# Kernel tuning notes

Measured on AMD Instinct MI355X. Metric: run time of the kernel, lower is better.

Reference implementation:

```python
import jax, jax.numpy as jnp
import numpy as np

EPS = 1e-6
NHEAD = 12

def _ln(x):
    m = jnp.mean(x, -1, keepdims=True)
    v = jnp.var(x, -1, keepdims=True)
    return (x - m) * jax.lax.rsqrt(v + EPS)

def _modulate(x, shift, scale):
    return x * (1 + scale[:, None, :]) + shift[:, None, :]

def _pos_embedding(idx, dim, max_len=2048):
    K = jnp.arange(dim // 2)
    ang = idx[..., None] * jnp.pi / (max_len ** (2.0 * K / dim))
    return jnp.concatenate([jnp.sin(ang), jnp.cos(ang)], axis=-1)

def _forward(x, W_xemb, b_xemb, ds_table, sg_table, Wqkv, bqkv, Wo, bo, W1, b1, W2, b2,
             Wada, bada, Wada_f, bada_f, W_out, dataset, spacegroup, mask):
    B, N, _ = x.shape
    D = W_xemb.shape[1]
    hd = D // NHEAD
    # conditioning vector: label embeddings (eval mode: no cfg dropout)
    c = ds_table[dataset] + sg_table[spacegroup]                 # [B, D]
    h = x @ W_xemb + b_xemb + _pos_embedding(jnp.arange(N), D)[None]  # [B, N, D]
    kmask = mask[:, None, None, :]                                # [B,1,1,N], True = padded key
    scale_qk = 1.0 / jnp.sqrt(jnp.asarray(hd, h.dtype))

    def block(h, p):
        Wqkv, bqkv, Wo, bo, W1, b1, W2, b2, Wada, bada = p
        mods = jax.nn.silu(c) @ Wada + bada                      # [B, 6D]
        sh_a, sc_a, g_a, sh_m, sc_m, g_m = jnp.split(mods, 6, axis=-1)
        xm = _modulate(_ln(h), sh_a, sc_a)
        qkv = (xm @ Wqkv + bqkv).reshape(B, N, 3, NHEAD, hd)
        q, k, v = qkv[:, :, 0], qkv[:, :, 1], qkv[:, :, 2]
        scores = jnp.einsum('bqhd,bkhd->bhqk', q, k) * scale_qk   # MATH-backend path: full [B,H,N,N]
        scores = jnp.where(kmask, -jnp.inf, scores)
        attn = jax.nn.softmax(scores, axis=-1)
        o = jnp.einsum('bhqk,bkhd->bqhd', attn, v).reshape(B, N, D)
        o = o @ Wo + bo
        h = h + g_a[:, None, :] * o
        y = _modulate(_ln(h), sh_m, sc_m)
        y = jax.nn.gelu(y @ W1 + b1, approximate=True) @ W2 + b2
        h = h + g_m[:, None, :] * y
        return h, None

    h, _ = jax.lax.scan(block, h, (Wqkv, bqkv, Wo, bo, W1, b1, W2, b2, Wada, bada))
    mods_f = jax.nn.silu(c) @ Wada_f + bada_f
    sh_f, sc_f = jnp.split(mods_f, 2, axis=-1)
    return _modulate(_ln(h), sh_f, sc_f) @ W_out                  # [B, N, 1] per-token energy


def setup_inputs() -> dict:
    B, N, D, L, DX, HID = 32, 512, 768, 12, 8, 3072
    keys = iter(jax.random.split(jax.random.key(0), 32))
    def w(shape, s=0.02):
        return jax.random.normal(next(keys), shape, jnp.float32) * s
    return dict(
        x=jax.random.normal(next(keys), (B, N, 2 * DX), jnp.float32),
        W_xemb=w((2 * DX, D)), b_xemb=jnp.zeros((D,), jnp.float32),
        ds_table=w((3, D)), sg_table=w((231, D)),
        Wqkv=w((L, D, 3 * D)), bqkv=jnp.zeros((L, 3 * D), jnp.float32),
        Wo=w((L, D, D)), bo=jnp.zeros((L, D), jnp.float32),
        W1=w((L, D, HID)), b1=jnp.zeros((L, HID), jnp.float32),
        W2=w((L, HID, D)), b2=jnp.zeros((L, D), jnp.float32),
        Wada=w((L, D, 6 * D)), bada=jnp.zeros((L, 6 * D), jnp.float32),
        Wada_f=w((D, 2 * D)), bada_f=jnp.zeros((2 * D,), jnp.float32),
        W_out=w((D, 1)),
        dataset=jax.random.randint(next(keys), (32,), 0, 2),
        spacegroup=jax.random.randint(next(keys), (32,), 0, 230),
        mask=jax.random.bernoulli(next(keys), 0.1, (32, 512)),
    )


def reference(x, W_xemb, b_xemb, ds_table, sg_table, Wqkv, bqkv, Wo, bo, W1, b1, W2, b2,
              Wada, bada, Wada_f, bada_f, W_out, dataset, spacegroup, mask):
    return _forward(x, W_xemb, b_xemb, ds_table, sg_table, Wqkv, bqkv, Wo, bo, W1, b1,
                    W2, b2, Wada, bada, Wada_f, bada_f, W_out, dataset, spacegroup, mask)
```

## Files before the change

### kernel.cpp

```cpp
#include <hip/hip_runtime.h>
#include <hip/hip_bf16.h>

#define B_   32
#define N_   512
#define D_   768
#define H_   12
#define HID_ 3072
#define L_   12
#define M_   (B_*N_)

typedef __attribute__((ext_vector_type(8))) short short8_t;
typedef __attribute__((ext_vector_type(4))) short short4_t;
typedef __attribute__((ext_vector_type(4))) float f32x4;
typedef __hip_bfloat16 bf16;

__device__ __forceinline__ void gll16(const void* g, void* l){
    __builtin_amdgcn_global_load_lds((const __attribute__((address_space(1))) void*)g,
                                     (__attribute__((address_space(3))) void*)l, 16, 0, 0);
}

__global__ __launch_bounds__(256) void embed_kernel(
    const float* __restrict__ x, const float* __restrict__ Wx,
    const float* __restrict__ bx, float* __restrict__ h)
{
    long idx = (long)blockIdx.x * 256 + threadIdx.x;
    int d = (int)(idx % 768);
    long m = idx / 768;
    int n = (int)(m % 512);
    float acc = bx[d];
    const float* xr = x + m * 16;
    #pragma unroll
    for (int k = 0; k < 16; ++k) acc = fmaf(xr[k], Wx[k*768 + d], acc);
    int K = (d < 384) ? d : d - 384;
    float ang = (float)n * 3.14159265358979323846f * expf(-(2.0f*(float)K/768.0f) * 7.624618986159398f);
    acc += (d < 384) ? sinf(ang) : cosf(ang);
    h[idx] = acc;
}

__global__ __launch_bounds__(256) void csilu_kernel(
    const float* __restrict__ ds_t, const float* __restrict__ sg_t,
    const int* __restrict__ dataset, const int* __restrict__ sg, float* __restrict__ out)
{
    int idx = blockIdx.x*256 + threadIdx.x;
    int b = idx / 768, d = idx % 768;
    float c = ds_t[dataset[b]*768 + d] + sg_t[sg[b]*768 + d];
    out[idx] = c / (1.0f + expf(-c));
}

__global__ __launch_bounds__(256) void mods_part_kernel(
    const float* __restrict__ csilu, const float* __restrict__ W,
    float* __restrict__ part, int Nd2, long wLayerStride)
{
    __shared__ float cs[16][96];
    int n2 = blockIdx.x*256 + threadIdx.x;
    int l = blockIdx.y, z = blockIdx.z;
    int kz = z >> 1, bg = z & 1;
    int L = gridDim.y;
    for (int t = threadIdx.x; t < 16*96; t += 256){
        int bb = t / 96, kk = t - bb*96;
        cs[bb][kk] = csilu[(bg*16 + bb)*768 + kz*96 + kk];
    }
    __syncthreads();
    const float2* Wl = (const float2*)(W + (long)l*wLayerStride);
    float2 acc[16];
    #pragma unroll
    for (int b=0;b<16;b++) acc[b] = make_float2(0.f, 0.f);
    for (int k=0;k<96;++k){
        float2 wv = Wl[(long)(kz*96 + k)*Nd2 + n2];
        #pragma unroll
        for (int b=0;b<16;b++){
            float c = cs[b][k];
            acc[b].x = fmaf(c, wv.x, acc[b].x);
            acc[b].y = fmaf(c, wv.y, acc[b].y);
        }
    }
    float2* pp = (float2*)part + ((long)(kz*L + l)*32 + bg*16)*Nd2 + n2;
    #pragma unroll
    for (int b=0;b<16;b++) pp[(long)b*Nd2] = acc[b];
}

__global__ __launch_bounds__(256) void mods_reduce_kernel(
    const float* __restrict__ part, const float* __restrict__ bias,
    float* __restrict__ out, int Nd, int L)
{
    long idx = (long)blockIdx.x*256 + threadIdx.x;
    int n = (int)(idx % Nd);
    long r = idx / Nd;
    int b = (int)(r & 31);
    int l = (int)(r >> 5);
    float s = bias[(long)l*Nd + n];
    #pragma unroll
    for (int z=0;z<8;z++) s += part[((long)(z*L + l)*32 + b)*Nd + n];
    out[idx] = s;
}

__global__ __launch_bounds__(256) void transpose4_kernel(
    const float* __restrict__ Wqkv, const float* __restrict__ Wo,
    const float* __restrict__ W1,  const float* __restrict__ W2,
    bf16* __restrict__ wqT, bf16* __restrict__ woT,
    bf16* __restrict__ w1T, bf16* __restrict__ w2T)
{
    __shared__ float t[32][33];
    int tt = blockIdx.x;
    const float* src; bf16* dst; int K, Nd, nx;
    if (tt < 1728){ src=Wqkv; dst=wqT; K=768; Nd=2304; nx=72; }
    else if (tt < 2304){ src=Wo; dst=woT; K=768; Nd=768; nx=24; tt -= 1728; }
    else if (tt < 4608){ src=W1; dst=w1T; K=768; Nd=3072; nx=96; tt -= 2304; }
    else { src=W2; dst=w2T; K=3072; Nd=768; nx=24; tt -= 4608; }
    int n0 = (tt % nx)*32, k0 = (tt / nx)*32;
    int tx = threadIdx.x & 31, ty = threadIdx.x >> 5;
    #pragma unroll
    for (int j=0;j<4;j++)
        t[ty + j*8][tx] = src[(long)(k0 + ty + j*8)*Nd + n0 + tx];
    __syncthreads();
    #pragma unroll
    for (int j=0;j<4;j++)
        dst[(long)(n0 + ty + j*8)*K + k0 + tx] = __float2bfloat16(t[tx][ty + j*8]);
}

__global__ __launch_bounds__(256) void ln_mod_kernel(
    const float* __restrict__ h, const float* __restrict__ shiftB,
    const float* __restrict__ scaleB, int modsStride, bf16* __restrict__ out)
{
    int wave = threadIdx.x >> 6, lane = threadIdx.x & 63;
    long row = (long)blockIdx.x*4 + wave;
    int b = (int)(row >> 9);
    const float4* xr = (const float4*)(h + row*768);
    float4 v[3];
    float s = 0.f, ss = 0.f;
    #pragma unroll
    for (int i=0;i<3;i++){
        v[i] = xr[lane + i*64];
        s  += v[i].x + v[i].y + v[i].z + v[i].w;
        ss += v[i].x*v[i].x + v[i].y*v[i].y + v[i].z*v[i].z + v[i].w*v[i].w;
    }
    #pragma unroll
    for (int o=1;o<64;o<<=1){ s += __shfl_xor(s,o,64); ss += __shfl_xor(ss,o,64); }
    float mean = s * (1.0f/768.0f);
    float var  = ss * (1.0f/768.0f) - mean*mean;
    float rstd = rsqrtf(var + 1e-6f);
    const float4* sh4 = (const float4*)(shiftB + (long)b*modsStride);
    const float4* sc4 = (const float4*)(scaleB + (long)b*modsStride);
    short4_t* orow = (short4_t*)(out + row*768);
    #pragma unroll
    for (int i=0;i<3;i++){
        float4 sh = sh4[lane + i*64];
        float4 sc = sc4[lane + i*64];
        float o0 = (v[i].x-mean)*rstd*(1.f+sc.x) + sh.x;
        float o1 = (v[i].y-mean)*rstd*(1.f+sc.y) + sh.y;
        float o2 = (v[i].z-mean)*rstd*(1.f+sc.z) + sh.z;
        float o3 = (v[i].w-mean)*rstd*(1.f+sc.w) + sh.w;
        bf16 b0 = __float2bfloat16(o0), b1 = __float2bfloat16(o1);
        bf16 b2 = __float2bfloat16(o2), b3 = __float2bfloat16(o3);
        short4_t pk;
        pk[0] = *(short*)&b0; pk[1] = *(short*)&b1;
        pk[2] = *(short*)&b2; pk[3] = *(short*)&b3;
        orow[lane + i*64] = pk;
    }
}

__device__ __forceinline__ float gelu_f(float x){
    float z2 = 1.5957691216057308f * x * (1.0f + 0.044715f*x*x);
    return x / (1.0f + __expf(-z2));
}

template<int MODE>
__global__ __launch_bounds__(256, 2) void gemm128_kernel(
    const bf16* __restrict__ A, const bf16* __restrict__ Bw,
    const float* __restrict__ bias, bf16* __restrict__ outBf,
    float* __restrict__ hres, const float* __restrict__ gate,
    int Nd, int Kd, int gateStride)
{
    __shared__ __align__(16) short lds[40960];
    int tid = threadIdx.x;
    int lane = tid & 63, wave = tid >> 6;
    int frow = lane & 15, g = lane >> 4;

    int nx = gridDim.x;
    int bid = blockIdx.y * nx + blockIdx.x;
    int xcd = bid & 7;
    int wq  = bid >> 3;
    int mt  = xcd * 16 + (wq & 15);
    int ct  = wq >> 4;
    int m0 = mt * 128, n0 = ct * 192;
    int wn = wave * 48;

    const short* Ag = (const short*)A;
    const short* Bg = (const short*)Bw;
    int r0 = tid >> 3, s0 = (tid & 7) ^ ((tid >> 3) & 7);
    const short* aSrc = Ag + (long)(m0 + r0)*Kd + s0*8;
    const short* bSrc = Bg + (long)(n0 + r0)*Kd + s0*8;
    long rj = (long)32*Kd;
    int wbase = wave*512;

    int aFrag = frow*64;
    int bFrag = (wn + frow)*64;
    int slotK0 = (g ^ (frow & 7))*8;
    int slotK1 = ((4+g) ^ (frow & 7))*8;

    f32x4 acc[8][3];
    #pragma unroll
    for (int i=0;i<8;i++)
        #pragma unroll
        for (int j=0;j<3;j++) acc[i][j] = (f32x4){0.f,0.f,0.f,0.f};

    int NT = Kd >> 6;

#define STAGE(kt, ps) { \
    int par_ = (kt)&1; \
    if ((ps)==0){ \
        short* d_ = &lds[par_*8192 + wbase]; \
        gll16(aSrc +        (long)(kt)*64, d_); \
        gll16(aSrc +   rj + (long)(kt)*64, d_ + 2048); \
        gll16(aSrc + 2*rj + (long)(kt)*64, d_ + 4096); \
        gll16(aSrc + 3*rj + (long)(kt)*64, d_ + 6144); \
    } else { \
        short* d_ = &lds[16384 + par_*12288 + wbase]; \
        gll16(bSrc +        (long)(kt)*64, d_); \
        gll16(bSrc +   rj + (long)(kt)*64, d_ + 2048); \
        gll16(bSrc + 2*rj + (long)(kt)*64, d_ + 4096); \
        gll16(bSrc + 3*rj + (long)(kt)*64, d_ + 6144); \
        gll16(bSrc + 4*rj + (long)(kt)*64, d_ + 8192); \
        gll16(bSrc + 5*rj + (long)(kt)*64, d_ + 10240); \
    } }

    STAGE(0,0); STAGE(0,1);

    for (int kt=0; kt<NT; ++kt){
        int pA  = (kt&1)*8192;
        int pBb = 16384 + (kt&1)*12288;
        bool pf = (kt+1 < NT);
        if (pf){
            STAGE(kt+1, 0);
            asm volatile("s_waitcnt vmcnt(4)" ::: "memory");
        } else {
            asm volatile("s_waitcnt vmcnt(0)" ::: "memory");
        }
        __builtin_amdgcn_s_barrier();
        __builtin_amdgcn_sched_barrier(0);
        if (pf) STAGE(kt+1, 1);
        short8_t af0[8], af1[8], bf0[3], bf1[3];
        #pragma unroll
        for (int i=0;i<8;i++){
            af0[i] = *(const short8_t*)&lds[pA + aFrag + i*1024 + slotK0];
            af1[i] = *(const short8_t*)&lds[pA + aFrag + i*1024 + slotK1];
        }
        #pragma unroll
        for (int j=0;j<3;j++){
            bf0[j] = *(const short8_t*)&lds[pBb + bFrag + j*1024 + slotK0];
            bf1[j] = *(const short8_t*)&lds[pBb + bFrag + j*1024 + slotK1];
        }
        __builtin_amdgcn_s_setprio(1);
        #pragma unroll
        for (int i=0;i<8;i++)
            #pragma unroll
            for (int j=0;j<3;j++)
                acc[i][j] = __builtin_amdgcn_mfma_f32_16x16x32_bf16(af0[i], bf0[j], acc[i][j], 0, 0, 0);
        #pragma unroll
        for (int i=0;i<8;i++)
            #pragma unroll
            for (int j=0;j<3;j++)
                acc[i][j] = __builtin_amdgcn_mfma_f32_16x16x32_bf16(af1[i], bf1[j], acc[i][j], 0, 0, 0);
        __builtin_amdgcn_s_setprio(0);
        __builtin_amdgcn_sched_barrier(0);
        __builtin_amdgcn_s_barrier();
        __builtin_amdgcn_sched_barrier(0);
    }
#undef STAGE

    int rbase = m0 + g*4;
    int cbase = n0 + wn + frow;
    float bv0 = bias[cbase], bv1 = bias[cbase+16], bv2 = bias[cbase+32];
    #pragma unroll
    for (int i=0;i<8;i++){
        #pragma unroll
        for (int r=0;r<4;r++){
            int row = rbase + i*16 + r;
            float v0 = acc[i][0][r] + bv0;
            float v1 = acc[i][1][r] + bv1;
            float v2 = acc[i][2][r] + bv2;
            if (MODE == 0){
                bf16* o_ = outBf + (long)row*Nd + cbase;
                o_[0]  = __float2bfloat16(v0);
                o_[16] = __float2bfloat16(v1);
                o_[32] = __float2bfloat16(v2);
            } else if (MODE == 1){
                bf16* o_ = outBf + (long)row*Nd + cbase;
                o_[0]  = __float2bfloat16(gelu_f(v0));
                o_[16] = __float2bfloat16(gelu_f(v1));
                o_[32] = __float2bfloat16(gelu_f(v2));
            } else {
                int bb = row >> 9;
                const float* gp = gate + (long)bb*gateStride + cbase;
                float* hp = hres + (long)row*768 + cbase;
                hp[0]  += gp[0]  * v0;
                hp[16] += gp[16] * v1;
                hp[32] += gp[32] * v2;
            }
        }
    }
}

__global__ __launch_bounds__(256) void attn_mfma_kernel(
    const bf16* __restrict__ qkv, const int* __restrict__ mask, bf16* __restrict__ o)
{
    __shared__ __align__(16) short Ks[64][72];
    __shared__ __align__(16) short Vt[64][72];
    __shared__ __align__(16) short Ps[4][16][72];
    __shared__ float maskf[512];
    int tid = threadIdx.x, lane = tid & 63, wave = tid >> 6;
    int qt = blockIdx.x, hh = blockIdx.y, b = blockIdx.z;
    long base = (long)b * 512 * 2304;
    const short* qkvs = (const short*)qkv;

    maskf[tid]       = mask[b*512 + tid]       ? -1e30f : 0.0f;
    maskf[tid + 256] = mask[b*512 + tid + 256] ? -1e30f : 0.0f;

    int c = lane & 15, g = lane >> 4;
    int qrowA = qt*64 + wave*16 + c;
    const short* qptr = qkvs + base + (long)qrowA*2304 + hh*64 + g*8;
    short8_t qa0 = *(const short8_t*)qptr;
    short8_t qa1 = *(const short8_t*)(qptr + 32);

    f32x4 oacc[4];
    #pragma unroll
    for (int j=0;j<4;j++) oacc[j] = (f32x4){0.f,0.f,0.f,0.f};
    float m_r[4], l_r[4];
    #pragma unroll
    for (int r=0;r<4;r++){ m_r[r] = -50.0f; l_r[r] = 0.0f; }

    int kp = (tid & 31)*2, gv = tid >> 5;
    const short* kgbase = qkvs + base + 768  + hh*64;
    const short* vgbase = qkvs + base + 1536 + hh*64 + gv*8;

    for (int kt=0; kt<8; ++kt){
        __syncthreads();
        {
            int v0 = tid, v1 = tid + 256;
            int r0 = v0>>3, c0 = (v0&7)*8, r1 = v1>>3, c1 = (v1&7)*8;
            *(short8_t*)&Ks[r0][c0] = *(const short8_t*)(kgbase + (long)(kt*64 + r0)*2304 + c0);
            *(short8_t*)&Ks[r1][c1] = *(const short8_t*)(kgbase + (long)(kt*64 + r1)*2304 + c1);
            short8_t va = *(const short8_t*)(vgbase + (long)(kt*64 + kp    )*2304);
            short8_t vb = *(const short8_t*)(vgbase + (long)(kt*64 + kp + 1)*2304);
            #pragma unroll
            for (int e=0;e<8;e++){
                unsigned int pack = (unsigned int)(unsigned short)va[e]
                                  | ((unsigned int)(unsigned short)vb[e] << 16);
                *(unsigned int*)&Vt[gv*8 + e][kp] = pack;
            }
        }
        __syncthreads();
        f32x4 s[4];
        #pragma unroll
        for (int j=0;j<4;j++){
            short8_t kb0 = *(const short8_t*)&Ks[j*16 + c][g*8];
            short8_t kb1 = *(const short8_t*)&Ks[j*16 + c][g*8 + 32];
            f32x4 z = (f32x4){0.f,0.f,0.f,0.f};
            z = __builtin_amdgcn_mfma_f32_16x16x32_bf16(qa0, kb0, z, 0, 0, 0);
            z = __builtin_amdgcn_mfma_f32_16x16x32_bf16(qa1, kb1, z, 0, 0, 0);
            s[j] = z;
        }
        #pragma unroll
        for (int j=0;j<4;j++){
            float mbj = maskf[kt*64 + j*16 + c];
            #pragma unroll
            for (int r=0;r<4;r++) s[j][r] = s[j][r]*0.125f + mbj;
        }
        #pragma unroll
        for (int r=0;r<4;r++){
            float tm = fmaxf(fmaxf(s[0][r], s[1][r]), fmaxf(s[2][r], s[3][r]));
            #pragma unroll
            for (int o_=1;o_<16;o_<<=1) tm = fmaxf(tm, __shfl_xor(tm, o_, 64));
            float mn  = fmaxf(m_r[r], tm);
            float fac = __expf(m_r[r] - mn);
            m_r[r] = mn;
            float ls = l_r[r]*fac;
            #pragma unroll
            for (int j=0;j<4;j++){
                float p = __expf(s[j][r] - mn);
                s[j][r] = p;
                ls += p;
            }
            l_r[r] = ls;
            #pragma unroll
            for (int j=0;j<4;j++) oacc[j][r] *= fac;
        }
        #pragma unroll
        for (int j=0;j<4;j++)
            #pragma unroll
            for (int r=0;r<4;r++)
                *(bf16*)&Ps[wave][g*4 + r][j*16 + c] = __float2bfloat16(s[j][r]);
        short8_t pa0 = *(const short8_t*)&Ps[wave][c][g*8];
        short8_t pa1 = *(const short8_t*)&Ps[wave][c][g*8 + 32];
        #pragma unroll
        for (int j=0;j<4;j++){
            short8_t vb0 = *(const short8_t*)&Vt[j*16 + c][g*8];
            short8_t vb1 = *(const short8_t*)&Vt[j*16 + c][g*8 + 32];
            oacc[j] = __builtin_amdgcn_mfma_f32_16x16x32_bf16(pa0, vb0, oacc[j], 0, 0, 0);
            oacc[j] = __builtin_amdgcn_mfma_f32_16x16x32_bf16(pa1, vb1, oacc[j], 0, 0, 0);
        }
    }
    #pragma unroll
    for (int r=0;r<4;r++){
        float lt = l_r[r];
        #pragma unroll
        for (int o_=1;o_<16;o_<<=1) lt += __shfl_xor(lt, o_, 64);
        l_r[r] = 1.0f / lt;
    }
    int qrowC = qt*64 + wave*16 + g*4;
    bf16* orow = o + ((long)b*512 + qrowC)*768 + hh*64;
    #pragma unroll
    for (int r=0;r<4;r++)
        #pragma unroll
        for (int j=0;j<4;j++)
            orow[(long)r*768 + j*16 + c] = __float2bfloat16(oacc[j][r] * l_r[r]);
}

__global__ __launch_bounds__(256) void outdot_kernel(
    const bf16* __restrict__ xm, const float* __restrict__ Wout, float* __restrict__ out)
{
    int tid=threadIdx.x, lane=tid&63, wave=tid>>6;
    long row = (long)blockIdx.x*4 + wave;
    const bf16* xr = xm + row*768;
    float acc = 0.f;
    #pragma unroll
    for (int i=0;i<12;i++){ int d = lane + i*64; acc = fmaf(__bfloat162float(xr[d]), Wout[d], acc); }
    #pragma unroll
    for (int o_=1;o_<64;o_<<=1) acc += __shfl_xor(acc, o_, 64);
    if (lane==0) out[row] = acc;
}

extern "C" void kernel_launch(void* const* d_in, const int* in_sizes, int n_in,
                              void* d_out, int out_size, void* d_ws, size_t ws_size,
                              hipStream_t stream)
{
    const float* x      = (const float*)d_in[0];
    const float* W_xemb = (const float*)d_in[1];
    const float* b_xemb = (const float*)d_in[2];
    const float* ds_t   = (const float*)d_in[3];
    const float* sg_t   = (const float*)d_in[4];
    const float* Wqkv   = (const float*)d_in[5];
    const float* bqkv   = (const float*)d_in[6];
    const float* Wo     = (const float*)d_in[7];
    const float* bo     = (const float*)d_in[8];
    const float* W1     = (const float*)d_in[9];
    const float* b1     = (const float*)d_in[10];
    const float* W2     = (const float*)d_in[11];
    const float* b2     = (const float*)d_in[12];
    const float* Wada   = (const float*)d_in[13];
    const float* bada   = (const float*)d_in[14];
    const float* Wada_f = (const float*)d_in[15];
    const float* bada_f = (const float*)d_in[16];
    const float* W_out  = (const float*)d_in[17];
    const int* dataset  = (const int*)d_in[18];
    const int* sgroup   = (const int*)d_in[19];
    const int* mask     = (const int*)d_in[20];
    float* out = (float*)d_out;

    char* ws = (char*)d_ws;
    size_t off = 0;
    auto alloc = [&](size_t bytes)->void*{
        void* p = ws + off; off += (bytes + 255) & ~(size_t)255; return p; };
    float* h     = (float*)alloc((size_t)M_*768*4);
    float* csilu = (float*)alloc((size_t)32*768*4);
    float* modsA = (float*)alloc((size_t)12*32*4608*4);
    float* modsF = (float*)alloc((size_t)32*1536*4);
    bf16*  xm    = (bf16*) alloc((size_t)M_*768*2);
    bf16*  wbuf  = (bf16*) alloc((size_t)7077888*2);
    bf16*  big   = (bf16*) alloc((size_t)M_*3072*2);
    bf16* qkvb = big;
    bf16* y1   = big;
    float* partA = (float*)big;
    float* partF = partA + (size_t)8*12*32*4608;
    bf16* wqT = wbuf;
    bf16* woT = wqT + 2304*768;
    bf16* w1T = woT + 768*768;
    bf16* w2T = w1T + 3072*768;

    embed_kernel<<<49152, 256, 0, stream>>>(x, W_xemb, b_xemb, h);
    csilu_kernel<<<96, 256, 0, stream>>>(ds_t, sg_t, dataset, sgroup, csilu);
    mods_part_kernel<<<dim3(9,12,16), 256, 0, stream>>>(csilu, Wada, partA, 2304, (long)768*4608);
    mods_reduce_kernel<<<6912, 256, 0, stream>>>(partA, bada, modsA, 4608, 12);
    mods_part_kernel<<<dim3(3,1,16), 256, 0, stream>>>(csilu, Wada_f, partF, 768, 0);
    mods_reduce_kernel<<<192, 256, 0, stream>>>(partF, bada_f, modsF, 1536, 1);

    for (int l=0; l<12; ++l){
        const float* modsL = modsA + (long)l*32*4608;
        transpose4_kernel<<<6912, 256, 0, stream>>>(
            Wqkv + (long)l*768*2304, Wo + (long)l*768*768,
            W1 + (long)l*768*3072,  W2 + (long)l*3072*768,
            wqT, woT, w1T, w2T);

        ln_mod_kernel<<<4096, 256, 0, stream>>>(h, modsL + 0*768, modsL + 1*768, 4608, xm);
        gemm128_kernel<0><<<dim3(12, 128), 256, 0, stream>>>(xm, wqT, bqkv + l*2304, qkvb,
                                                             nullptr, nullptr, 2304, 768, 0);
        attn_mfma_kernel<<<dim3(8, 12, 32), 256, 0, stream>>>(qkvb, mask, xm);
        gemm128_kernel<2><<<dim3(4, 128), 256, 0, stream>>>(xm, woT, bo + l*768, nullptr,
                                                            h, modsL + 2*768, 768, 768, 4608);
        ln_mod_kernel<<<4096, 256, 0, stream>>>(h, modsL + 3*768, modsL + 4*768, 4608, xm);
        gemm128_kernel<1><<<dim3(16, 128), 256, 0, stream>>>(xm, w1T, b1 + l*3072, y1,
                                                             nullptr, nullptr, 3072, 768, 0);
        gemm128_kernel<2><<<dim3(4, 128), 256, 0, stream>>>(y1, w2T, b2 + l*768, nullptr,
                                                            h, modsL + 5*768, 768, 3072, 4608);
    }
    ln_mod_kernel<<<4096, 256, 0, stream>>>(h, modsF + 0, modsF + 768, 1536, xm);
    outdot_kernel<<<4096, 256, 0, stream>>>(xm, W_out, out);
}
```

Baseline: 4.680 ms.

## Add 256x128-tile 512-thread GEMM with triple-buffered LDS for QKV and FFN1

Adds a new bf16 MFMA GEMM kernel that computes 256x128 output tiles with 8 waves. A tiles are triple-buffered and B tiles double-buffered in LDS, loaded through global_load_lds with an XOR swizzle, and the MFMAs run at raised wave priority. Block indices are remapped so that neighbouring M tiles land on the same XCD. The QKV projection and the first FFN GEMM (with gelu) now use it, with the aim of raising data reuse and overlapping loads with compute compared with the 128-tile kernel. It uses about 128KB of LDS per block, so only one block fits per CU, and it assumes the dimensions divide evenly.

Result: slower. 5.160 ms (+10.2%).

```diff
diff --git a/kernel.cpp b/kernel.cpp
--- a/kernel.cpp
+++ b/kernel.cpp
@@ -301,6 +301,122 @@
     }
 }
 
+template<int MODE>
+__global__ __launch_bounds__(512, 1) void gemm256x128_kernel(
+    const bf16* __restrict__ A, const bf16* __restrict__ Bw,
+    const float* __restrict__ bias, bf16* __restrict__ outBf,
+    int Nd, int Kd)
+{
+    __shared__ __align__(16) short lds[65536];
+    int tid = threadIdx.x;
+    int lane = tid & 63, wave = tid >> 6;
+    int frow = lane & 15, g = lane >> 4;
+    int wm = wave >> 1, wn = wave & 1;
+
+    int bid = blockIdx.x;
+    int xcd = bid & 7, wq = bid >> 3;
+    int mt = xcd*8 + (wq & 7);
+    int ct = wq >> 3;
+    int m0 = mt*256, n0 = ct*128;
+
+    const short* Ag = (const short*)A;
+    const short* Bg = (const short*)Bw;
+    int r0 = tid >> 3, s0 = (tid & 7) ^ (r0 & 7);
+    const short* aSrc = Ag + (long)(m0 + r0)*Kd + s0*8;
+    const short* bSrc = Bg + (long)(n0 + r0)*Kd + s0*8;
+    long r64 = (long)64*Kd;
+    int wb = wave*512;
+
+    int aRd = (wm*64 + frow)*64;
+    int bRd = (wn*64 + frow)*64;
+    int slotK0 = (g ^ (frow & 7))*8;
+    int slotK1 = ((4+g) ^ (frow & 7))*8;
+
+    f32x4 acc[4][4];
+    #pragma unroll
+    for (int i=0;i<4;i++)
+        #pragma unroll
+        for (int j=0;j<4;j++) acc[i][j] = (f32x4){0.f,0.f,0.f,0.f};
+
+    int NT = Kd >> 6;
+
+#define STA2(kt, qq) { \
+    short* dA_ = &lds[((kt)%3)*16384 + (qq)*4096 + wb]; \
+    const short* sA_ = aSrc + (long)(qq)*r64 + (long)(kt)*64; \
+    gll16(sA_, dA_); gll16(sA_ + r64, dA_ + 4096); }
+#define STB(kt) { \
+    short* dB_ = &lds[49152 + ((kt)&1)*8192 + wb]; \
+    const short* sB_ = bSrc + (long)(kt)*64; \
+    gll16(sB_, dB_); gll16(sB_ + r64, dB_ + 4096); }
+
+    STA2(0,0); STA2(0,2); STB(0); STA2(1,0); STA2(1,2);
+    asm volatile("s_waitcnt vmcnt(4)" ::: "memory");
+    __builtin_amdgcn_s_barrier();
+    __builtin_amdgcn_sched_barrier(0);
+
+    for (int kt=0; kt<NT; ++kt){
+        int pA = (kt%3)*16384;
+        int pB = 49152 + (kt&1)*8192;
+        bool p1 = (kt+1 < NT), p2 = (kt+2 < NT);
+
+        short8_t af[4], bfr[4];
+        #pragma unroll
+        for (int i=0;i<4;i++) af[i]  = *(const short8_t*)&lds[pA + aRd + i*1024 + slotK0];
+        #pragma unroll
+        for (int j=0;j<4;j++) bfr[j] = *(const short8_t*)&lds[pB + bRd + j*1024 + slotK0];
+        if (p1) STB(kt+1);
+        if (p2) STA2(kt+2, 0);
+        __builtin_amdgcn_s_setprio(1);
+        #pragma unroll
+        for (int i=0;i<4;i++)
+            #pragma unroll
+            for (int j=0;j<4;j++)
+                acc[i][j] = __builtin_amdgcn_mfma_f32_16x16x32_bf16(af[i], bfr[j], acc[i][j], 0, 0, 0);
+        __builtin_amdgcn_s_setprio(0);
+        #pragma unroll
+        for (int i=0;i<4;i++) af[i]  = *(const short8_t*)&lds[pA + aRd + i*1024 + slotK1];
+        #pragma unroll
+        for (int j=0;j<4;j++) bfr[j] = *(const short8_t*)&lds[pB + bRd + j*1024 + slotK1];
+        if (p2) STA2(kt+2, 2);
+        __builtin_amdgcn_s_setprio(1);
+        #pragma unroll
+        for (int i=0;i<4;i++)
+            #pragma unroll
+            for (int j=0;j<4;j++)
+                acc[i][j] = __builtin_amdgcn_mfma_f32_16x16x32_bf16(af[i], bfr[j], acc[i][j], 0, 0, 0);
+        __builtin_amdgcn_s_setprio(0);
+        __builtin_amdgcn_sched_barrier(0);
+        if (p2)      { asm volatile("s_waitcnt vmcnt(4)" ::: "memory"); }
+        else if (p1) { asm volatile("s_waitcnt vmcnt(0)" ::: "memory"); }
+        if (p1){
+            __builtin_amdgcn_s_barrier();
+            __builtin_amdgcn_sched_barrier(0);
+        }
+    }
+#undef STA2
+#undef STB
+
+    int rb = m0 + wm*64 + g*4;
+    int cb = n0 + wn*64 + frow;
+    float bv[4];
+    #pragma unroll
+    for (int j=0;j<4;j++) bv[j] = bias[cb + j*16];
+    #pragma unroll
+    for (int i=0;i<4;i++){
+        #pragma unroll
+        for (int r=0;r<4;r++){
+            int row = rb + i*16 + r;
+            bf16* o_ = outBf + (long)row*Nd + cb;
+            #pragma unroll
+            for (int j=0;j<4;j++){
+                float v = acc[i][j][r] + bv[j];
+                if (MODE == 1) v = gelu_f(v);
+                o_[j*16] = __float2bfloat16(v);
+            }
+        }
+    }
+}
+
 __global__ __launch_bounds__(256) void attn_mfma_kernel(
     const bf16* __restrict__ qkv, const int* __restrict__ mask, bf16* __restrict__ o)
 {
@@ -492,14 +608,12 @@
             wqT, woT, w1T, w2T);
 
         ln_mod_kernel<<<4096, 256, 0, stream>>>(h, modsL + 0*768, modsL + 1*768, 4608, xm);
-        gemm128_kernel<0><<<dim3(12, 128), 256, 0, stream>>>(xm, wqT, bqkv + l*2304, qkvb,
-                                                             nullptr, nullptr, 2304, 768, 0);
+        gemm256x128_kernel<0><<<1152, 512, 0, stream>>>(xm, wqT, bqkv + l*2304, qkvb, 2304, 768);
         attn_mfma_kernel<<<dim3(8, 12, 32), 256, 0, stream>>>(qkvb, mask, xm);
         gemm128_kernel<2><<<dim3(4, 128), 256, 0, stream>>>(xm, woT, bo + l*768, nullptr,
                                                             h, modsL + 2*768, 768, 768, 4608);
         ln_mod_kernel<<<4096, 256, 0, stream>>>(h, modsL + 3*768, modsL + 4*768, 4608, xm);
-        gemm128_kernel<1><<<dim3(16, 128), 256, 0, stream>>>(xm, w1T, b1 + l*3072, y1,
-                                                             nullptr, nullptr, 3072, 768, 0);
+        gemm256x128_kernel<1><<<1536, 512, 0, stream>>>(xm, w1T, b1 + l*3072, y1, 3072, 768);
         gemm128_kernel<2><<<dim3(4, 128), 256, 0, stream>>>(y1, w2T, b2 + l*768, nullptr,
                                                             h, modsL + 5*768, 768, 3072, 4608);
     }
```

## Double-buffer K/V tiles in attention and precompute positional table

Applied to the files above, without the earlier changes.

The attention kernel now prefetches the next K/V tile into registers while computing the current one, then writes it into a second LDS buffer. This drops one barrier per iteration and hides global load latency. Separately, the sin/cos positional embedding is computed once into a 512x768 table instead of per batch element in the embed kernel. The cost is doubled LDS for K/V, which may reduce occupancy, plus extra live registers.

New measurement: 4.671 ms. Within noise of the previous version (-0.2%).

```diff
diff --git a/kernel.cpp b/kernel.cpp
--- a/kernel.cpp
+++ b/kernel.cpp
@@ -19,21 +19,28 @@
                                      (__attribute__((address_space(3))) void*)l, 16, 0, 0);
 }
 
+__global__ __launch_bounds__(256) void pos_kernel(float* __restrict__ ptab)
+{
+    int idx = blockIdx.x*256 + threadIdx.x;
+    int d = idx % 768, n = idx / 768;
+    int K = (d < 384) ? d : d - 384;
+    float ang = (float)n * 3.14159265358979323846f * expf(-(2.0f*(float)K/768.0f) * 7.624618986159398f);
+    ptab[idx] = (d < 384) ? sinf(ang) : cosf(ang);
+}
+
 __global__ __launch_bounds__(256) void embed_kernel(
     const float* __restrict__ x, const float* __restrict__ Wx,
-    const float* __restrict__ bx, float* __restrict__ h)
+    const float* __restrict__ bx, const float* __restrict__ ptab,
+    float* __restrict__ h)
 {
     long idx = (long)blockIdx.x * 256 + threadIdx.x;
     int d = (int)(idx % 768);
     long m = idx / 768;
     int n = (int)(m % 512);
-    float acc = bx[d];
+    float acc = bx[d] + ptab[n*768 + d];
     const float* xr = x + m * 16;
     #pragma unroll
     for (int k = 0; k < 16; ++k) acc = fmaf(xr[k], Wx[k*768 + d], acc);
-    int K = (d < 384) ? d : d - 384;
-    float ang = (float)n * 3.14159265358979323846f * expf(-(2.0f*(float)K/768.0f) * 7.624618986159398f);
-    acc += (d < 384) ? sinf(ang) : cosf(ang);
     h[idx] = acc;
 }
 
@@ -304,8 +311,8 @@
 __global__ __launch_bounds__(256) void attn_mfma_kernel(
     const bf16* __restrict__ qkv, const int* __restrict__ mask, bf16* __restrict__ o)
 {
-    __shared__ __align__(16) short Ks[64][72];
-    __shared__ __align__(16) short Vt[64][72];
+    __shared__ __align__(16) short Ks[2][64][72];
+    __shared__ __align__(16) short Vt[2][64][72];
     __shared__ __align__(16) short Ps[4][16][72];
     __shared__ float maskf[512];
     int tid = threadIdx.x, lane = tid & 63, wave = tid >> 6;
@@ -333,28 +340,36 @@
     const short* kgbase = qkvs + base + 768  + hh*64;
     const short* vgbase = qkvs + base + 1536 + hh*64 + gv*8;
 
+    int r0s = tid >> 3, c0s = (tid & 7)*8;
+    int r1s = r0s + 32;
+
+    short8_t ka, kb2, va, vb;
+#define LDREGS(kt) { \
+    ka  = *(const short8_t*)(kgbase + (long)((kt)*64 + r0s)*2304 + c0s); \
+    kb2 = *(const short8_t*)(kgbase + (long)((kt)*64 + r1s)*2304 + c0s); \
+    va  = *(const short8_t*)(vgbase + (long)((kt)*64 + kp    )*2304); \
+    vb  = *(const short8_t*)(vgbase + (long)((kt)*64 + kp + 1)*2304); }
+#define WRLDS(bf_) { \
+    *(short8_t*)&Ks[bf_][r0s][c0s] = ka; \
+    *(short8_t*)&Ks[bf_][r1s][c0s] = kb2; \
+    _Pragma("unroll") \
+    for (int e=0;e<8;e++){ \
+        unsigned int pack = (unsigned int)(unsigned short)va[e] \
+                          | ((unsigned int)(unsigned short)vb[e] << 16); \
+        *(unsigned int*)&Vt[bf_][gv*8 + e][kp] = pack; } }
+
+    LDREGS(0);
+    WRLDS(0);
+    __syncthreads();
+
     for (int kt=0; kt<8; ++kt){
-        __syncthreads();
-        {
-            int v0 = tid, v1 = tid + 256;
-            int r0 = v0>>3, c0 = (v0&7)*8, r1 = v1>>3, c1 = (v1&7)*8;
-            *(short8_t*)&Ks[r0][c0] = *(const short8_t*)(kgbase + (long)(kt*64 + r0)*2304 + c0);
-            *(short8_t*)&Ks[r1][c1] = *(const short8_t*)(kgbase + (long)(kt*64 + r1)*2304 + c1);
-            short8_t va = *(const short8_t*)(vgbase + (long)(kt*64 + kp    )*2304);
-            short8_t vb = *(const short8_t*)(vgbase + (long)(kt*64 + kp + 1)*2304);
-            #pragma unroll
-            for (int e=0;e<8;e++){
-                unsigned int pack = (unsigned int)(unsigned short)va[e]
-                                  | ((unsigned int)(unsigned short)vb[e] << 16);
-                *(unsigned int*)&Vt[gv*8 + e][kp] = pack;
-            }
-        }
-        __syncthreads();
+        int cb = kt & 1;
+        if (kt < 7) LDREGS(kt+1);
         f32x4 s[4];
         #pragma unroll
         for (int j=0;j<4;j++){
-            short8_t kb0 = *(const short8_t*)&Ks[j*16 + c][g*8];
-            short8_t kb1 = *(const short8_t*)&Ks[j*16 + c][g*8 + 32];
+            short8_t kb0 = *(const short8_t*)&Ks[cb][j*16 + c][g*8];
+            short8_t kb1 = *(const short8_t*)&Ks[cb][j*16 + c][g*8 + 32];
             f32x4 z = (f32x4){0.f,0.f,0.f,0.f};
             z = __builtin_amdgcn_mfma_f32_16x16x32_bf16(qa0, kb0, z, 0, 0, 0);
             z = __builtin_amdgcn_mfma_f32_16x16x32_bf16(qa1, kb1, z, 0, 0, 0);
@@ -394,12 +409,20 @@
         short8_t pa1 = *(const short8_t*)&Ps[wave][c][g*8 + 32];
         #pragma unroll
         for (int j=0;j<4;j++){
-            short8_t vb0 = *(const short8_t*)&Vt[j*16 + c][g*8];
-            short8_t vb1 = *(const short8_t*)&Vt[j*16 + c][g*8 + 32];
+            short8_t vb0 = *(const short8_t*)&Vt[cb][j*16 + c][g*8];
+            short8_t vb1 = *(const short8_t*)&Vt[cb][j*16 + c][g*8 + 32];
             oacc[j] = __builtin_amdgcn_mfma_f32_16x16x32_bf16(pa0, vb0, oacc[j], 0, 0, 0);
             oacc[j] = __builtin_amdgcn_mfma_f32_16x16x32_bf16(pa1, vb1, oacc[j], 0, 0, 0);
         }
-    }
+        if (kt < 7){
+            asm volatile("s_waitcnt vmcnt(0)" ::: "memory");
+            WRLDS(cb ^ 1);
+        }
+        __syncthreads();
+    }
+#undef LDREGS
+#undef WRLDS
+
     #pragma unroll
     for (int r=0;r<4;r++){
         float lt = l_r[r];
@@ -465,6 +488,7 @@
     float* csilu = (float*)alloc((size_t)32*768*4);
     float* modsA = (float*)alloc((size_t)12*32*4608*4);
     float* modsF = (float*)alloc((size_t)32*1536*4);
+    float* ptab  = (float*)alloc((size_t)512*768*4);
     bf16*  xm    = (bf16*) alloc((size_t)M_*768*2);
     bf16*  wbuf  = (bf16*) alloc((size_t)7077888*2);
     bf16*  big   = (bf16*) alloc((size_t)M_*3072*2);
@@ -477,7 +501,8 @@
     bf16* w1T = woT + 768*768;
     bf16* w2T = w1T + 3072*768;
 
-    embed_kernel<<<49152, 256, 0, stream>>>(x, W_xemb, b_xemb, h);
+    pos_kernel<<<1536, 256, 0, stream>>>(ptab);
+    embed_kernel<<<49152, 256, 0, stream>>>(x, W_xemb, b_xemb, ptab, h);
     csilu_kernel<<<96, 256, 0, stream>>>(ds_t, sg_t, dataset, sgroup, csilu);
     mods_part_kernel<<<dim3(9,12,16), 256, 0, stream>>>(csilu, Wada, partA, 2304, (long)768*4608);
     mods_reduce_kernel<<<6912, 256, 0, stream>>>(partA, bada, modsA, 4608, 12);
```
